# Kernel tuning notes

Hardware: AMD Instinct MI355X
Metric: run time of the kernel (lower is better)

The kernel has to match this reference:

```python
import jax, jax.numpy as jnp
import numpy as np

EPS = 1e-5  # matches scipy Rbf smooth and the jitter scale in the torch module


def _phi_r2(r2):
    # thin-plate basis r^2 * log(r) = 0.5 * r2 * log(r2), with phi(0)=0 (scipy xlogy)
    safe = jnp.where(r2 > 0, r2, 1.0)
    return jnp.where(r2 > 0, 0.5 * safe * jnp.log(safe), 0.0)


def _bilinear(im, x, y):
    # im: [C,H,W]; x,y: [H,W] sample coords (already clipped to valid range)
    H, W = im.shape[1], im.shape[2]
    xf, yf = jnp.floor(x), jnp.floor(y)
    x0 = jnp.clip(xf.astype(jnp.int32), 0, W - 1)
    x1 = jnp.clip((xf + 1.0).astype(jnp.int32), 0, W - 1)
    y0 = jnp.clip(yf.astype(jnp.int32), 0, H - 1)
    y1 = jnp.clip((yf + 1.0).astype(jnp.int32), 0, H - 1)
    Ia = im[:, y0, x0]
    Ib = im[:, y1, x0]
    Ic = im[:, y0, x1]
    Id = im[:, y1, x1]
    wa = (x1 - x) * (y1 - y)
    wb = (x1 - x) * (y - y0)
    wc = (x - x0) * (y1 - y)
    wd = (x - x0) * (y - y0)
    return wa * Ia + wb * Ib + wc * Ic + wd * Id


def setup_inputs() -> dict:
    key = jax.random.key(0)
    k1, k2, k3 = jax.random.split(key, 3)
    B, C, H, W, N = 16, 3, 512, 384, 18
    cloth_image = jax.random.normal(k1, (B, C, H, W), dtype=jnp.float32)
    # keypoints in pixel coordinates: x in [0, W-1], y in [0, H-1]
    kp01 = jax.random.uniform(k2, (B, N, 2), dtype=jnp.float32)
    keypoints = kp01 * jnp.array([W - 1.0, H - 1.0], dtype=jnp.float32)
    control_points = jax.random.normal(k3, (N, 2), dtype=jnp.float32)
    return {"cloth_image": cloth_image, "keypoints": keypoints, "control_points": control_points}


def reference(cloth_image, keypoints, control_points):
    B, C, H, W = cloth_image.shape
    N = control_points.shape[0]
    # deterministic stand-in for the epsilon * randn jitter on dst points
    jitter = EPS * jax.random.normal(jax.random.key(1), keypoints.shape, dtype=keypoints.dtype)
    dst = keypoints + jitter                                  # [B,N,2] (x,y)
    src = jnp.broadcast_to(control_points[None], (B, N, 2))    # [B,N,2]

    # ---- batched TPS solve (scipy Rbf: A = phi(r_ij) - smooth*I; nodes = A^{-1} d) ----
    d2 = jnp.sum((dst[:, :, None, :] - dst[:, None, :, :]) ** 2, axis=-1)  # [B,N,N]
    A = _phi_r2(d2) - EPS * jnp.eye(N, dtype=dst.dtype)
    nodes = jnp.linalg.solve(A, src)                           # [B,N,2] -> (nodes_x, nodes_y)

    # ---- evaluate warp on the full pixel grid ----
    gx, gy = jnp.meshgrid(jnp.arange(W, dtype=cloth_image.dtype),
                          jnp.arange(H, dtype=cloth_image.dtype))
    grid = jnp.stack([gx.ravel(), gy.ravel()], axis=-1)        # [P,2], P=H*W
    # squared distances grid<->dst via expansion (avoids [B,P,N,2] intermediate)
    g2 = jnp.sum(grid ** 2, axis=-1)                           # [P]
    p2 = jnp.sum(dst ** 2, axis=-1)                            # [B,N]
    cross = jnp.einsum('pk,bnk->bpn', grid, dst)               # [B,P,N]
    r2 = jnp.maximum(g2[None, :, None] + p2[:, None, :] - 2.0 * cross, 0.0)
    warped = jnp.einsum('bpn,bnk->bpk', _phi_r2(r2), nodes)    # [B,P,2]
    wx = jnp.clip(warped[..., 0], 0.0, W - 1.0).reshape(B, H, W)
    wy = jnp.clip(warped[..., 1], 0.0, H - 1.0).reshape(B, H, W)

    # ---- batched bilinear sampling ----
    warped_cloth = jax.vmap(_bilinear)(cloth_image, wx, wy)    # [B,C,H,W]
    return warped_cloth
```

## Files before the change

kernel.cpp:

```cpp
#include <hip/hip_runtime.h>
#include <math.h>

constexpr int B = 16, C = 3, H = 512, W = 384, N = 18;
constexpr int HW = H * W;

using v2f = __attribute__((ext_vector_type(2))) float;

__device__ __forceinline__ unsigned rotl32(unsigned x, int d) {
    return (x << d) | (x >> (32 - d));
}

__device__ void threefry2x32_01(unsigned c0, unsigned c1, unsigned& o0, unsigned& o1) {
    const unsigned ks0 = 0u, ks1 = 1u, ks2 = 0x1BD11BDBu;
    unsigned x0 = c0 + ks0;
    unsigned x1 = c1 + ks1;
#define R4(a,b,c,d)                               \
    x0 += x1; x1 = rotl32(x1,(a)); x1 ^= x0;      \
    x0 += x1; x1 = rotl32(x1,(b)); x1 ^= x0;      \
    x0 += x1; x1 = rotl32(x1,(c)); x1 ^= x0;      \
    x0 += x1; x1 = rotl32(x1,(d)); x1 ^= x0;
    R4(13,15,26,6)   x0 += ks1; x1 += ks2 + 1u;
    R4(17,29,16,24)  x0 += ks2; x1 += ks0 + 2u;
    R4(13,15,26,6)   x0 += ks0; x1 += ks1 + 3u;
    R4(17,29,16,24)  x0 += ks1; x1 += ks2 + 4u;
    R4(13,15,26,6)   x0 += ks2; x1 += ks0 + 5u;
#undef R4
    o0 = x0; o1 = x1;
}

__global__ __launch_bounds__(64) void solve_kernel(
        const float* __restrict__ keypoints,
        const float* __restrict__ control_points,
        float* __restrict__ params) {
    const int b = blockIdx.x;
    const int tid = threadIdx.x;
    __shared__ float dstx[N], dsty[N];
    __shared__ double Ab[N][21];

    if (tid < 2 * N) {
        const int e = b * 2 * N + tid;
        const unsigned lo = (e < 288) ? (unsigned)e : (unsigned)(e - 288);
        unsigned o0, o1;
        threefry2x32_01(lo, lo + 288u, o0, o1);
        const unsigned bits = (e < 288) ? o0 : o1;
        const float f = __uint_as_float(0x3F800000u | (bits >> 9)) - 1.0f;
        const float lof = __uint_as_float(0xBF7FFFFFu);
        const float span = __uint_as_float(0x3FFFFFFFu);
        float u = f * span + lof;
        u = fmaxf(u, lof);
        const float nrm = 1.41421356f * erfinvf(u);
        const float v = keypoints[e] + 1e-5f * nrm;
        if ((tid & 1) == 0) dstx[tid >> 1] = v; else dsty[tid >> 1] = v;
    }
    __syncthreads();

    for (int idx = tid; idx < N * N; idx += 64) {
        const int i = idx / N, j = idx % N;
        const double dx = (double)dstx[i] - (double)dstx[j];
        const double dy = (double)dsty[i] - (double)dsty[j];
        const double d2 = dx * dx + dy * dy;
        const double phi = (d2 > 0.0) ? 0.5 * d2 * log(d2) : 0.0;
        Ab[i][j] = phi - (i == j ? 1e-5 : 0.0);
    }
    if (tid < 2 * N) {
        Ab[tid >> 1][18 + (tid & 1)] = (double)control_points[tid];
    }
    __syncthreads();

    for (int k = 0; k < N; ++k) {
        double v = (tid >= k && tid < N) ? fabs(Ab[tid][k]) : -1.0;
        int idxl = tid;
#pragma unroll
        for (int off = 16; off >= 1; off >>= 1) {
            const double ov = __shfl_xor(v, off);
            const int oi = __shfl_xor(idxl, off);
            if (ov > v) { v = ov; idxl = oi; }
        }
        const int p = __shfl(idxl, 0);
        if (p != k && tid < 20) {
            const double t = Ab[k][tid]; Ab[k][tid] = Ab[p][tid]; Ab[p][tid] = t;
        }
        __syncthreads();
        const double inv = 1.0 / Ab[k][k];
        if (tid < N && tid != k) {
            const double m = Ab[tid][k] * inv;
#pragma unroll
            for (int j = 0; j < 20; ++j) Ab[tid][j] -= m * Ab[k][j];
        }
        __syncthreads();
    }

    float* pb = params + b * 72;
    if (tid < N) {
        pb[tid]      = dstx[tid];
        pb[18 + tid] = dsty[tid];
        const double sc = 0.34657359027997264;
        pb[36 + tid] = (float)(sc * Ab[tid][18] / Ab[tid][tid]);
        pb[54 + tid] = (float)(sc * Ab[tid][19] / Ab[tid][tid]);
    }
}

__global__ __launch_bounds__(256) void warp_kernel(
        const float* __restrict__ image,
        const float* __restrict__ params,
        float* __restrict__ out) {
    constexpr int PPB = 512;
    constexpr int BPB = HW / PPB;
    const int blk = blockIdx.x;
    const int b = blk / BPB;
    const int pix0 = (blk - b * BPB) * PPB + threadIdx.x * 2;
    const int y = pix0 / W;
    const int x = pix0 - y * W;

    const float* __restrict__ pb = params + b * 72;
    const float py = (float)y;
    const v2f px = { (float)x, (float)(x + 1) };
    v2f ax = { 0.f, 0.f }, ay = { 0.f, 0.f };
#pragma unroll
    for (int n = 0; n < N; ++n) {
        const float kx = pb[n];
        const float ky = pb[18 + n];
        const float nx = pb[36 + n];
        const float ny = pb[54 + n];
        const v2f dx = px - kx;
        const float dy = py - ky;
        const float dy2 = dy * dy;
        v2f r2 = dx * dx + dy2;
        r2.x = fmaxf(r2.x, 1e-30f);
        r2.y = fmaxf(r2.y, 1e-30f);
        v2f lg;
        lg.x = __builtin_amdgcn_logf(r2.x);
        lg.y = __builtin_amdgcn_logf(r2.y);
        const v2f phi = r2 * lg;
        ax += phi * nx;
        ay += phi * ny;
    }

    const float* imb = image + (size_t)b * C * HW;
    float* outb = out + (size_t)b * C * HW;
    v2f o0, o1, o2;
#pragma unroll
    for (int j = 0; j < 2; ++j) {
        const float wx = fminf(fmaxf(ax[j], 0.f), (float)(W - 1));
        const float wy = fminf(fmaxf(ay[j], 0.f), (float)(H - 1));
        const float xf = floorf(wx), yf = floorf(wy);
        const int x0 = min(max((int)xf, 0), W - 1);
        const int x1 = min(max((int)(xf + 1.f), 0), W - 1);
        const int y0 = min(max((int)yf, 0), H - 1);
        const int y1 = min(max((int)(yf + 1.f), 0), H - 1);
        const float wa = ((float)x1 - wx) * ((float)y1 - wy);
        const float wb = ((float)x1 - wx) * (wy - (float)y0);
        const float wc = (wx - (float)x0) * ((float)y1 - wy);
        const float wd = (wx - (float)x0) * (wy - (float)y0);
        const int ia = y0 * W + x0, ib = y1 * W + x0;
        const int ic = y0 * W + x1, id = y1 * W + x1;
        {
            const float* ch = imb;
            o0[j] = wa * ch[ia] + wb * ch[ib] + wc * ch[ic] + wd * ch[id];
        }
        {
            const float* ch = imb + HW;
            o1[j] = wa * ch[ia] + wb * ch[ib] + wc * ch[ic] + wd * ch[id];
        }
        {
            const float* ch = imb + 2 * HW;
            o2[j] = wa * ch[ia] + wb * ch[ib] + wc * ch[ic] + wd * ch[id];
        }
    }
    *reinterpret_cast<v2f*>(outb + pix0) = o0;
    *reinterpret_cast<v2f*>(outb + HW + pix0) = o1;
    *reinterpret_cast<v2f*>(outb + 2 * HW + pix0) = o2;
}

extern "C" void kernel_launch(void* const* d_in, const int* in_sizes, int n_in,
                              void* d_out, int out_size, void* d_ws, size_t ws_size,
                              hipStream_t stream) {
    const float* cloth     = (const float*)d_in[0];
    const float* keypoints = (const float*)d_in[1];
    const float* ctrl      = (const float*)d_in[2];
    float* params = (float*)d_ws;

    solve_kernel<<<B, 64, 0, stream>>>(keypoints, ctrl, params);
    warp_kernel<<<(B * HW) / 512, 256, 0, stream>>>(cloth, params, (float*)d_out);
}
```

Measured before the change: 48.24 us.

## Register-resident Gauss-Jordan solve, 4 pixels per thread, XCD-aware block swizzle

The solve kernel now keeps each matrix row in registers and does Gauss-Jordan elimination with wave shuffles and implicit pivoting. This removes the shared-memory row swaps and the two barriers per pivot step. The warp kernel processes four pixels per thread with 128-bit stores and half as many blocks. Block indices are swizzled across groups of eight, presumably to spread batches across XCDs for cache locality. Register pressure rises with the wider vectors, and the solve path changes pivot bookkeeping.

```diff
diff --git a/kernel.cpp b/kernel.cpp
--- a/kernel.cpp
+++ b/kernel.cpp
@@ -4,7 +4,7 @@
 constexpr int B = 16, C = 3, H = 512, W = 384, N = 18;
 constexpr int HW = H * W;
 
-using v2f = __attribute__((ext_vector_type(2))) float;
+using v4f = __attribute__((ext_vector_type(4))) float;
 
 __device__ __forceinline__ unsigned rotl32(unsigned x, int d) {
     return (x << d) | (x >> (32 - d));
@@ -35,7 +35,7 @@
     const int b = blockIdx.x;
     const int tid = threadIdx.x;
     __shared__ float dstx[N], dsty[N];
-    __shared__ double Ab[N][21];
+    __shared__ double Ab[N][20];
 
     if (tid < 2 * N) {
         const int e = b * 2 * N + tid;
@@ -54,49 +54,60 @@
     }
     __syncthreads();
 
-    for (int idx = tid; idx < N * N; idx += 64) {
-        const int i = idx / N, j = idx % N;
-        const double dx = (double)dstx[i] - (double)dstx[j];
-        const double dy = (double)dsty[i] - (double)dsty[j];
-        const double d2 = dx * dx + dy * dy;
-        const double phi = (d2 > 0.0) ? 0.5 * d2 * log(d2) : 0.0;
-        Ab[i][j] = phi - (i == j ? 1e-5 : 0.0);
-    }
-    if (tid < 2 * N) {
-        Ab[tid >> 1][18 + (tid & 1)] = (double)control_points[tid];
+    for (int idx = tid; idx < N * 20; idx += 64) {
+        const int i = idx / 20, j = idx - (idx / 20) * 20;
+        double v;
+        if (j < N) {
+            const double dx = (double)dstx[i] - (double)dstx[j];
+            const double dy = (double)dsty[i] - (double)dsty[j];
+            const double d2 = dx * dx + dy * dy;
+            const double phi = (d2 > 0.0) ? 0.5 * d2 * log(d2) : 0.0;
+            v = phi - (i == j ? 1e-5 : 0.0);
+        } else {
+            v = (double)control_points[2 * i + (j - N)];
+        }
+        Ab[i][j] = v;
     }
     __syncthreads();
 
+    const int row = min(tid, N - 1);
+    double a[20];
+#pragma unroll
+    for (int j = 0; j < 20; ++j) a[j] = Ab[row][j];
+
+    bool used = (tid >= N);
+    double invs = 0.0;
+    int myvar = -1;
+
+#pragma unroll
     for (int k = 0; k < N; ++k) {
-        double v = (tid >= k && tid < N) ? fabs(Ab[tid][k]) : -1.0;
-        int idxl = tid;
+        double cand = used ? -1.0 : fabs(a[k]);
+        int il = tid;
 #pragma unroll
-        for (int off = 16; off >= 1; off >>= 1) {
-            const double ov = __shfl_xor(v, off);
-            const int oi = __shfl_xor(idxl, off);
-            if (ov > v) { v = ov; idxl = oi; }
+        for (int off = 32; off >= 1; off >>= 1) {
+            const double oc = __shfl_xor(cand, off);
+            const int oi = __shfl_xor(il, off);
+            if (oc > cand || (oc == cand && oi < il)) { cand = oc; il = oi; }
         }
-        const int p = __shfl(idxl, 0);
-        if (p != k && tid < 20) {
-            const double t = Ab[k][tid]; Ab[k][tid] = Ab[p][tid]; Ab[p][tid] = t;
+        const int p = __shfl(il, 0);
+        const double piv = __shfl(a[k], p);
+        const double inv = 1.0 / piv;
+        const bool iam = (tid == p);
+        if (iam) { used = true; myvar = k; invs = inv; }
+        const double m = iam ? 0.0 : a[k] * inv;
+#pragma unroll
+        for (int j = k + 1; j < 20; ++j) {
+            const double prj = __shfl(a[j], p);
+            a[j] = fma(-m, prj, a[j]);
         }
-        __syncthreads();
-        const double inv = 1.0 / Ab[k][k];
-        if (tid < N && tid != k) {
-            const double m = Ab[tid][k] * inv;
-#pragma unroll
-            for (int j = 0; j < 20; ++j) Ab[tid][j] -= m * Ab[k][j];
-        }
-        __syncthreads();
     }
 
     float* pb = params + b * 72;
-    if (tid < N) {
-        pb[tid]      = dstx[tid];
-        pb[18 + tid] = dsty[tid];
+    if (tid < N) { pb[tid] = dstx[tid]; pb[18 + tid] = dsty[tid]; }
+    if (myvar >= 0) {
         const double sc = 0.34657359027997264;
-        pb[36 + tid] = (float)(sc * Ab[tid][18] / Ab[tid][tid]);
-        pb[54 + tid] = (float)(sc * Ab[tid][19] / Ab[tid][tid]);
+        pb[36 + myvar] = (float)(sc * a[18] * invs);
+        pb[54 + myvar] = (float)(sc * a[19] * invs);
     }
 }
 
@@ -104,43 +115,46 @@
         const float* __restrict__ image,
         const float* __restrict__ params,
         float* __restrict__ out) {
-    constexpr int PPB = 512;
+    constexpr int PPB = 1024;
     constexpr int BPB = HW / PPB;
-    const int blk = blockIdx.x;
-    const int b = blk / BPB;
-    const int pix0 = (blk - b * BPB) * PPB + threadIdx.x * 2;
+    constexpr int NBLK = B * BPB;
+    const int bid = blockIdx.x;
+    const int swz = (bid & 7) * (NBLK / 8) + (bid >> 3);
+    const int b = swz / BPB;
+    const int pix0 = (swz - b * BPB) * PPB + threadIdx.x * 4;
     const int y = pix0 / W;
     const int x = pix0 - y * W;
 
     const float* __restrict__ pb = params + b * 72;
     const float py = (float)y;
-    const v2f px = { (float)x, (float)(x + 1) };
-    v2f ax = { 0.f, 0.f }, ay = { 0.f, 0.f };
+    const v4f px = { (float)x, (float)(x + 1), (float)(x + 2), (float)(x + 3) };
+    v4f ax = { 0.f, 0.f, 0.f, 0.f }, ay = { 0.f, 0.f, 0.f, 0.f };
 #pragma unroll
     for (int n = 0; n < N; ++n) {
         const float kx = pb[n];
         const float ky = pb[18 + n];
         const float nx = pb[36 + n];
         const float ny = pb[54 + n];
-        const v2f dx = px - kx;
         const float dy = py - ky;
         const float dy2 = dy * dy;
-        v2f r2 = dx * dx + dy2;
-        r2.x = fmaxf(r2.x, 1e-30f);
-        r2.y = fmaxf(r2.y, 1e-30f);
-        v2f lg;
-        lg.x = __builtin_amdgcn_logf(r2.x);
-        lg.y = __builtin_amdgcn_logf(r2.y);
-        const v2f phi = r2 * lg;
+        const v4f dx = px - kx;
+        v4f r2 = dx * dx + dy2;
+        v4f lg;
+#pragma unroll
+        for (int j = 0; j < 4; ++j) {
+            r2[j] = fmaxf(r2[j], 1e-30f);
+            lg[j] = __builtin_amdgcn_logf(r2[j]);
+        }
+        const v4f phi = r2 * lg;
         ax += phi * nx;
         ay += phi * ny;
     }
 
     const float* imb = image + (size_t)b * C * HW;
     float* outb = out + (size_t)b * C * HW;
-    v2f o0, o1, o2;
+    v4f o0, o1, o2;
 #pragma unroll
-    for (int j = 0; j < 2; ++j) {
+    for (int j = 0; j < 4; ++j) {
         const float wx = fminf(fmaxf(ax[j], 0.f), (float)(W - 1));
         const float wy = fminf(fmaxf(ay[j], 0.f), (float)(H - 1));
         const float xf = floorf(wx), yf = floorf(wy);
@@ -154,22 +168,15 @@
         const float wd = (wx - (float)x0) * (wy - (float)y0);
         const int ia = y0 * W + x0, ib = y1 * W + x0;
         const int ic = y0 * W + x1, id = y1 * W + x1;
-        {
-            const float* ch = imb;
-            o0[j] = wa * ch[ia] + wb * ch[ib] + wc * ch[ic] + wd * ch[id];
-        }
-        {
-            const float* ch = imb + HW;
-            o1[j] = wa * ch[ia] + wb * ch[ib] + wc * ch[ic] + wd * ch[id];
-        }
-        {
-            const float* ch = imb + 2 * HW;
-            o2[j] = wa * ch[ia] + wb * ch[ib] + wc * ch[ic] + wd * ch[id];
-        }
+        o0[j] = wa * imb[ia] + wb * imb[ib] + wc * imb[ic] + wd * imb[id];
+        const float* c1 = imb + HW;
+        o1[j] = wa * c1[ia] + wb * c1[ib] + wc * c1[ic] + wd * c1[id];
+        const float* c2 = imb + 2 * HW;
+        o2[j] = wa * c2[ia] + wb * c2[ib] + wc * c2[ic] + wd * c2[id];
     }
-    *reinterpret_cast<v2f*>(outb + pix0) = o0;
-    *reinterpret_cast<v2f*>(outb + HW + pix0) = o1;
-    *reinterpret_cast<v2f*>(outb + 2 * HW + pix0) = o2;
+    *reinterpret_cast<v4f*>(outb + pix0) = o0;
+    *reinterpret_cast<v4f*>(outb + HW + pix0) = o1;
+    *reinterpret_cast<v4f*>(outb + 2 * HW + pix0) = o2;
 }
 
 extern "C" void kernel_launch(void* const* d_in, const int* in_sizes, int n_in,
@@ -181,5 +188,5 @@
     float* params = (float*)d_ws;
 
     solve_kernel<<<B, 64, 0, stream>>>(keypoints, ctrl, params);
-    warp_kernel<<<(B * HW) / 512, 256, 0, stream>>>(cloth, params, (float*)d_out);
+    warp_kernel<<<(B * HW) / 1024, 256, 0, stream>>>(cloth, params, (float*)d_out);
 }
```

After: 44.85 us. 1.08x faster.
